# Optimization experiments

Hardware: AMD Instinct MI355X
Metric: run time of the kernel (lower is better)

The kernel has to match this reference:

```python
import jax, jax.numpy as jnp
import numpy as np


def silu(v):
    return v * jax.nn.sigmoid(v)


def setup_inputs() -> dict:
    key = jax.random.key(0)
    ks = jax.random.split(key, 10)
    b, l, d_model = 1, 1024, 1536
    d_inner, dt_rank, d_state, d_conv = 3072, 96, 16, 4
    rn = lambda k, shp, sc: jax.random.normal(k, shp, jnp.float32) * sc
    return {
        "hidden_states": rn(ks[0], (b, l, d_model), 1.0),
        "in_proj_w": rn(ks[1], (2 * d_inner, d_model), 0.02),
        "conv_w": rn(ks[2], (d_inner, d_conv), 0.1),
        "conv_b": rn(ks[3], (d_inner,), 0.1),
        "x_proj_w": rn(ks[4], (dt_rank + 2 * d_state, d_inner), 0.02),
        "dt_proj_w": rn(ks[5], (d_inner, dt_rank), 0.02),
        "dt_proj_b": rn(ks[6], (d_inner,), 0.1),
        "out_proj_w": rn(ks[7], (d_model, d_inner), 0.02),
        "A_log": jnp.log(jax.random.uniform(ks[8], (d_inner, d_state), jnp.float32, 0.5, 8.0)),
        "D": rn(ks[9], (d_inner,), 1.0),
    }


def reference(hidden_states, in_proj_w, conv_w, conv_b, x_proj_w, dt_proj_w, dt_proj_b, out_proj_w, A_log, D):
    b, l, _ = hidden_states.shape
    d_inner, d_conv = conv_w.shape
    dt_rank = dt_proj_w.shape[1]
    d_state = A_log.shape[1]
    negA = -jnp.exp(A_log)  # (d_inner, d_state)

    # in_proj, transpose to channel-major: (b, 2*d_inner, l)
    xz = jnp.einsum('bld,ed->ble', hidden_states, in_proj_w).transpose(0, 2, 1)
    x, z = jnp.split(xz, 2, axis=1)  # each (b, d_inner, l)

    # conv_state = F.pad(x, (d_conv - l, 0)) -> last d_conv columns (l > d_conv)
    conv_state = x[:, :, -d_conv:]

    # causal depthwise conv1d + bias + silu
    xp = jnp.pad(x, ((0, 0), (0, 0), (d_conv - 1, 0)))
    xc = conv_b[None, :, None] + sum(conv_w[None, :, j:j + 1] * xp[:, :, j:j + l] for j in range(d_conv))
    xc = silu(xc)  # (b, d_inner, l)

    # x_proj over channel dim -> dt, B, C
    x_dbl = jnp.einsum('bdl,ed->ble', xc, x_proj_w)  # (b, l, dt_rank+2*d_state)
    dt, Bm, Cm = jnp.split(x_dbl, [dt_rank, dt_rank + d_state], axis=-1)

    # dt_proj (no bias here; bias folded into softplus as delta_bias)
    delta = jax.nn.softplus(jnp.einsum('blr,dr->bdl', dt, dt_proj_w) + dt_proj_b[None, :, None])

    # selective scan: h_t = exp(delta_t * A) * h_{t-1} + delta_t * B_t * x_t
    deltaA = jnp.exp(delta[..., None] * negA[None, :, None, :])          # (b, d, l, n)
    deltaBx = delta[..., None] * Bm[:, None, :, :] * xc[..., None]        # (b, d, l, n)

    def comb(c1, c2):
        a1, u1 = c1
        a2, u2 = c2
        return a1 * a2, a2 * u1 + u2

    _, h = jax.lax.associative_scan(comb, (deltaA, deltaBx), axis=2)      # (b, d, l, n)

    y = jnp.einsum('bdln,bln->bdl', h, Cm) + D[None, :, None] * xc
    y = y * silu(z)

    out = jnp.einsum('bdl,od->blo', y, out_proj_w)  # (b, l, d_model)
    last_state = h[:, :, -1, :]                     # (b, d_inner, d_state)
    return out, conv_state, last_state
```

## Files before the change

kernel.cpp:

```cpp
#include <hip/hip_runtime.h>

using f32x4  = __attribute__((ext_vector_type(4))) float;
using bf16x4 = __attribute__((ext_vector_type(4))) __bf16;
using bf16x8 = __attribute__((ext_vector_type(8))) __bf16;

#define L_SEQ 1024
#define D_MODEL 1536
#define D_INNER 3072
#define DT_RANK 96
#define D_STATE 16

#define SCAN_NC 32
#define SCAN_CL (L_SEQ / SCAN_NC)
#define NCHAIN  (D_INNER * D_STATE)

#define SCRATCH_FLOATS (4 * L_SEQ * D_INNER + L_SEQ * 128 + 3 * SCAN_NC * NCHAIN)
__device__ __align__(16) float g_scratch[SCRATCH_FLOATS];

template <int BM, int BN, int BK, int AMODE, int BMODE, int EPI, int SWZY = 0>
__global__ __launch_bounds__(256) void gemm_bt(
    const float* __restrict__ Ap, const float* __restrict__ Bp,
    float* __restrict__ out0, float* __restrict__ out1,
    const float* __restrict__ bias,
    int M, int N, int K, int lda, int ldb, int ldc)
{
    constexpr int LDSK = BK + 8;
    constexpr int WM = BM / 2, WN = BN / 2;
    constexpr int FM = WM / 16, FN = WN / 16;
    constexpr int CHA = (BM * BK / 256) / 4;
    constexpr int CHB = (BN * BK / 256) / 4;
    constexpr int CPR = BK / 4;
    __shared__ __align__(16) __bf16 As [BM * LDSK];
    __shared__ __align__(16) __bf16 As2[(AMODE == 2) ? BM * LDSK : 8];
    __shared__ __align__(16) __bf16 Bs [BN * LDSK];
    __shared__ __align__(16) __bf16 Bs2[(BMODE == 2) ? BN * LDSK : 8];

    const int tid  = threadIdx.x;
    const int lane = tid & 63;
    const int wid  = tid >> 6;
    const int wm = wid >> 1, wn = wid & 1;

    int m0, n0;
    if constexpr (SWZY > 0) {
        int b   = blockIdx.x;
        int xcd = b & 7;
        int j   = b >> 3;
        m0 = (j / SWZY) * BM;
        n0 = (xcd * SWZY + (j % SWZY)) * BN;
    } else {
        m0 = blockIdx.x * BM;
        n0 = blockIdx.y * BN;
    }

    const int nkt = (K + BK - 1) / BK;
    const int per = (nkt + (int)gridDim.z - 1) / (int)gridDim.z;
    const int kb  = blockIdx.z * per * BK;
    const int ke  = min(K, kb + per * BK);

    f32x4 acc[FM][FN];
#pragma unroll
    for (int i = 0; i < FM; ++i)
#pragma unroll
        for (int j = 0; j < FN; ++j) acc[i][j] = f32x4{0.f, 0.f, 0.f, 0.f};

    const int fr = lane & 15, kq = lane >> 4;

    f32x4 a0[CHA], a1[CHA], b0[CHB], b1[CHB];

    auto loadAb = [&](int kt, f32x4 (&buf)[CHA]) {
#pragma unroll
        for (int i = 0; i < CHA; ++i) {
            int c = i * 256 + tid;
            int r = c / CPR, k4 = c % CPR;
            buf[i] = *(const f32x4*)(Ap + (size_t)(m0 + r) * lda + kt + k4 * 4);
        }
    };
    auto loadBb = [&](int kt, f32x4 (&buf)[CHB]) {
#pragma unroll
        for (int i = 0; i < CHB; ++i) {
            int c = i * 256 + tid;
            int r = c / CPR, k4 = c % CPR;
            buf[i] = *(const f32x4*)(Bp + (size_t)(n0 + r) * ldb + kt + k4 * 4);
        }
    };
    auto writeAb = [&](f32x4 (&buf)[CHA]) {
#pragma unroll
        for (int i = 0; i < CHA; ++i) {
            int c = i * 256 + tid;
            int r = c / CPR, k4 = c % CPR;
            bf16x4 hv;
#pragma unroll
            for (int e = 0; e < 4; ++e) hv[e] = (__bf16)buf[i][e];
            *(bf16x4*)&As[r * LDSK + k4 * 4] = hv;
            if constexpr (AMODE == 2) {
                bf16x4 lv;
#pragma unroll
                for (int e = 0; e < 4; ++e)
                    lv[e] = (__bf16)(buf[i][e] - (float)hv[e]);
                *(bf16x4*)&As2[r * LDSK + k4 * 4] = lv;
            }
        }
    };
    auto writeBb = [&](f32x4 (&buf)[CHB]) {
#pragma unroll
        for (int i = 0; i < CHB; ++i) {
            int c = i * 256 + tid;
            int r = c / CPR, k4 = c % CPR;
            bf16x4 hv;
#pragma unroll
            for (int e = 0; e < 4; ++e) hv[e] = (__bf16)buf[i][e];
            *(bf16x4*)&Bs[r * LDSK + k4 * 4] = hv;
            if constexpr (BMODE == 2) {
                bf16x4 lv;
#pragma unroll
                for (int e = 0; e < 4; ++e)
                    lv[e] = (__bf16)(buf[i][e] - (float)hv[e]);
                *(bf16x4*)&Bs2[r * LDSK + k4 * 4] = lv;
            }
        }
    };
    auto compute = [&]() {
        bf16x8 af[FM], bfg[FN];
#pragma unroll
        for (int fm = 0; fm < FM; ++fm)
            af[fm] = *(const bf16x8*)&As[(wm * WM + fm * 16 + fr) * LDSK + kq * 8];
#pragma unroll
        for (int fn = 0; fn < FN; ++fn)
            bfg[fn] = *(const bf16x8*)&Bs[(wn * WN + fn * 16 + fr) * LDSK + kq * 8];
        if constexpr (AMODE == 2 && BMODE == 2) {
            bf16x8 al[FM], bl[FN];
#pragma unroll
            for (int fm = 0; fm < FM; ++fm)
                al[fm] = *(const bf16x8*)&As2[(wm * WM + fm * 16 + fr) * LDSK + kq * 8];
#pragma unroll
            for (int fn = 0; fn < FN; ++fn)
                bl[fn] = *(const bf16x8*)&Bs2[(wn * WN + fn * 16 + fr) * LDSK + kq * 8];
#pragma unroll
            for (int fm = 0; fm < FM; ++fm)
#pragma unroll
                for (int fn = 0; fn < FN; ++fn) {
                    acc[fm][fn] = __builtin_amdgcn_mfma_f32_16x16x32_bf16(
                        al[fm], bfg[fn], acc[fm][fn], 0, 0, 0);
                    acc[fm][fn] = __builtin_amdgcn_mfma_f32_16x16x32_bf16(
                        af[fm], bl[fn], acc[fm][fn], 0, 0, 0);
                    acc[fm][fn] = __builtin_amdgcn_mfma_f32_16x16x32_bf16(
                        af[fm], bfg[fn], acc[fm][fn], 0, 0, 0);
                }
        } else {
#pragma unroll
            for (int fm = 0; fm < FM; ++fm)
#pragma unroll
                for (int fn = 0; fn < FN; ++fn)
                    acc[fm][fn] = __builtin_amdgcn_mfma_f32_16x16x32_bf16(
                        af[fm], bfg[fn], acc[fm][fn], 0, 0, 0);
        }
    };

    loadAb(kb, a0);
    loadBb(kb, b0);
    if (kb + BK < ke) {
        loadAb(kb + BK, a1);
        loadBb(kb + BK, b1);
    }

    for (int kt = kb; kt < ke; kt += 2 * BK) {
        writeAb(a0);
        writeBb(b0);
        __syncthreads();
        if (kt + 2 * BK < ke) {
            loadAb(kt + 2 * BK, a0);
            loadBb(kt + 2 * BK, b0);
        }
        compute();
        __syncthreads();
        if (kt + BK < ke) {
            writeAb(a1);
            writeBb(b1);
            __syncthreads();
            if (kt + 3 * BK < ke) {
                loadAb(kt + 3 * BK, a1);
                loadBb(kt + 3 * BK, b1);
            }
            compute();
            __syncthreads();
        }
    }

    const int rbase = m0 + wm * WM, cbase = n0 + wn * WN;
#pragma unroll
    for (int fm = 0; fm < FM; ++fm) {
#pragma unroll
        for (int fn = 0; fn < FN; ++fn) {
            int row = rbase + fm * 16 + (lane >> 4) * 4;
            int col = cbase + fn * 16 + (lane & 15);
            f32x4 v = acc[fm][fn];
            if (EPI == 0) {
                int split = N / 2;
                float* d = (col < split) ? out0 : out1;
                int cc = (col < split) ? col : col - split;
#pragma unroll
                for (int j = 0; j < 4; ++j) d[(size_t)(row + j) * ldc + cc] = v[j];
            } else if (EPI == 1) {
                float bz = bias[col];
#pragma unroll
                for (int j = 0; j < 4; ++j) {
                    float t = v[j] + bz;
                    t = (t > 20.f) ? t : log1pf(__expf(t));
                    out0[(size_t)(row + j) * ldc + col] = t;
                }
            } else if (EPI == 2) {
#pragma unroll
                for (int j = 0; j < 4; ++j)
                    atomicAdd(&out0[(size_t)(row + j) * ldc + col], v[j]);
            } else if (EPI == 3) {
#pragma unroll
                for (int j = 0; j < 4; ++j)
                    out0[(size_t)(row + j) * ldc + col] = v[j];
            } else if (EPI == 4) {
                float* d = out0 + (size_t)blockIdx.z * M * ldc;
#pragma unroll
                for (int j = 0; j < 4; ++j)
                    d[(size_t)(row + j) * ldc + col] = v[j];
            } else {
#pragma unroll
                for (int j = 0; j < 4; ++j) {
                    float t = v[j] + bias[row + j];
                    t = (t > 20.f) ? t : log1pf(__expf(t));
                    out0[(size_t)(row + j) * ldc + col] = t;
                }
            }
        }
    }
}

__global__ __launch_bounds__(256) void zero_f32(float* __restrict__ p, int n4)
{
    int i = blockIdx.x * 256 + threadIdx.x;
    if (i < n4) ((f32x4*)p)[i] = f32x4{0.f, 0.f, 0.f, 0.f};
}

__global__ __launch_bounds__(256) void reduce2_f32(
    const float* __restrict__ p, float* __restrict__ out, int n4)
{
    int i = blockIdx.x * 256 + threadIdx.x;
    if (i < n4) {
        f32x4 a = ((const f32x4*)p)[i];
        f32x4 b = ((const f32x4*)(p + (size_t)L_SEQ * D_MODEL))[i];
        ((f32x4*)out)[i] = a + b;
    }
}

__global__ __launch_bounds__(256) void conv_silu(
    const float* __restrict__ x, const float* __restrict__ cw,
    const float* __restrict__ cb, float* __restrict__ xc,
    float* __restrict__ conv_state)
{
    int idx = blockIdx.x * 256 + threadIdx.x;
    int l  = idx / (D_INNER / 4);
    int d4 = (idx % (D_INNER / 4)) * 4;
    const f32x4 zero = f32x4{0.f, 0.f, 0.f, 0.f};
    f32x4 x0 = *(const f32x4*)&x[(size_t)l * D_INNER + d4];
    f32x4 x1 = (l >= 1) ? *(const f32x4*)&x[(size_t)(l - 1) * D_INNER + d4] : zero;
    f32x4 x2 = (l >= 2) ? *(const f32x4*)&x[(size_t)(l - 2) * D_INNER + d4] : zero;
    f32x4 x3 = (l >= 3) ? *(const f32x4*)&x[(size_t)(l - 3) * D_INNER + d4] : zero;
    f32x4 r;
#pragma unroll
    for (int i = 0; i < 4; ++i) {
        int d = d4 + i;
        float w0 = cw[d * 4 + 0], w1 = cw[d * 4 + 1];
        float w2 = cw[d * 4 + 2], w3 = cw[d * 4 + 3];
        float v = cb[d] + w3 * x0[i] + w2 * x1[i] + w1 * x2[i] + w0 * x3[i];
        r[i] = v / (1.f + __expf(-v));
    }
    *(f32x4*)&xc[(size_t)l * D_INNER + d4] = r;
    if (l == L_SEQ - 1) {
#pragma unroll
        for (int i = 0; i < 4; ++i) {
            int d = d4 + i;
            conv_state[d * 4 + 3] = x0[i];
            conv_state[d * 4 + 2] = x1[i];
            conv_state[d * 4 + 1] = x2[i];
            conv_state[d * 4 + 0] = x3[i];
        }
    }
}

__global__ __launch_bounds__(256) void scan_phase1(
    const float* __restrict__ delta, const float* __restrict__ xc,
    const float* __restrict__ dbl, const float* __restrict__ A_log,
    float* __restrict__ U, float* __restrict__ Aprod)
{
    int d = blockIdx.x * 256 + threadIdx.x;
    int c = blockIdx.y;
    float a[D_STATE], h[D_STATE], p[D_STATE];
#pragma unroll
    for (int n = 0; n < D_STATE; n += 4) {
        f32x4 av = *(const f32x4*)&A_log[d * D_STATE + n];
#pragma unroll
        for (int e = 0; e < 4; ++e) {
            a[n + e] = __expf(av[e]);
            h[n + e] = 0.f;
            p[n + e] = 1.f;
        }
    }
    int l0 = c * SCAN_CL;
    for (int i = 0; i < SCAN_CL; ++i) {
        int l = l0 + i;
        float dl = delta[(size_t)l * D_INNER + d];
        float xv = xc[(size_t)l * D_INNER + d];
        const float* Bp = dbl + l * 128 + DT_RANK;
        f32x4 B0 = *(const f32x4*)(Bp);
        f32x4 B1 = *(const f32x4*)(Bp + 4);
        f32x4 B2 = *(const f32x4*)(Bp + 8);
        f32x4 B3 = *(const f32x4*)(Bp + 12);
        float dx = dl * xv;
#pragma unroll
        for (int n = 0; n < D_STATE; ++n) {
            float Bv = (n < 4) ? B0[n] : (n < 8) ? B1[n - 4]
                     : (n < 12) ? B2[n - 8] : B3[n - 12];
            float dA = __expf(-dl * a[n]);
            h[n] = fmaf(dA, h[n], dx * Bv);
            p[n] *= dA;
        }
    }
    size_t base = (size_t)c * NCHAIN + (size_t)d * D_STATE;
#pragma unroll
    for (int n = 0; n < D_STATE; n += 4) {
        *(f32x4*)&U[base + n]     = f32x4{h[n], h[n+1], h[n+2], h[n+3]};
        *(f32x4*)&Aprod[base + n] = f32x4{p[n], p[n+1], p[n+2], p[n+3]};
    }
}

__global__ __launch_bounds__(256) void scan_phase2(
    const float* __restrict__ U, const float* __restrict__ Aprod,
    float* __restrict__ Hin, float* __restrict__ last_state)
{
    int r = blockIdx.x * 256 + threadIdx.x;
    float hin = 0.f;
#pragma unroll
    for (int c = 0; c < SCAN_NC; ++c) {
        Hin[c * NCHAIN + r] = hin;
        hin = fmaf(Aprod[c * NCHAIN + r], hin, U[c * NCHAIN + r]);
    }
    last_state[r] = hin;
}

__global__ __launch_bounds__(256) void scan_phase3(
    const float* __restrict__ delta, const float* __restrict__ xc,
    const float* __restrict__ z, const float* __restrict__ dbl,
    const float* __restrict__ A_log, const float* __restrict__ Dp,
    const float* __restrict__ Hin, float* __restrict__ y)
{
    int d = blockIdx.x * 256 + threadIdx.x;
    int c = blockIdx.y;
    float a[D_STATE], h[D_STATE];
    size_t hbase = (size_t)c * NCHAIN + (size_t)d * D_STATE;
#pragma unroll
    for (int n = 0; n < D_STATE; n += 4) {
        f32x4 av = *(const f32x4*)&A_log[d * D_STATE + n];
        f32x4 hv = *(const f32x4*)&Hin[hbase + n];
#pragma unroll
        for (int e = 0; e < 4; ++e) {
            a[n + e] = __expf(av[e]);
            h[n + e] = hv[e];
        }
    }
    float Dv = Dp[d];
    int l0 = c * SCAN_CL;
    for (int i = 0; i < SCAN_CL; ++i) {
        int l = l0 + i;
        float dl = delta[(size_t)l * D_INNER + d];
        float xv = xc[(size_t)l * D_INNER + d];
        float zv = z[(size_t)l * D_INNER + d];
        const float* Bp = dbl + l * 128 + DT_RANK;
        f32x4 B0 = *(const f32x4*)(Bp);
        f32x4 B1 = *(const f32x4*)(Bp + 4);
        f32x4 B2 = *(const f32x4*)(Bp + 8);
        f32x4 B3 = *(const f32x4*)(Bp + 12);
        f32x4 C0 = *(const f32x4*)(Bp + 16);
        f32x4 C1 = *(const f32x4*)(Bp + 20);
        f32x4 C2 = *(const f32x4*)(Bp + 24);
        f32x4 C3 = *(const f32x4*)(Bp + 28);
        float dx = dl * xv;
        float yv = 0.f;
#pragma unroll
        for (int n = 0; n < D_STATE; ++n) {
            float Bv = (n < 4) ? B0[n] : (n < 8) ? B1[n - 4]
                     : (n < 12) ? B2[n - 8] : B3[n - 12];
            float Cv = (n < 4) ? C0[n] : (n < 8) ? C1[n - 4]
                     : (n < 12) ? C2[n - 8] : C3[n - 12];
            float dA = __expf(-dl * a[n]);
            h[n] = fmaf(dA, h[n], dx * Bv);
            yv = fmaf(h[n], Cv, yv);
        }
        float sz = zv / (1.f + __expf(-zv));
        y[(size_t)l * D_INNER + d] = (yv + Dv * xv) * sz;
    }
}

extern "C" void kernel_launch(void* const* d_in, const int* in_sizes, int n_in,
                              void* d_out, int out_size, void* d_ws, size_t ws_size,
                              hipStream_t stream)
{
    const float* hs    = (const float*)d_in[0];
    const float* Win   = (const float*)d_in[1];
    const float* cw    = (const float*)d_in[2];
    const float* cb    = (const float*)d_in[3];
    const float* Wx    = (const float*)d_in[4];
    const float* Wdt   = (const float*)d_in[5];
    const float* dtb   = (const float*)d_in[6];
    const float* Wout  = (const float*)d_in[7];
    const float* A_log = (const float*)d_in[8];
    const float* Dp    = (const float*)d_in[9];

    float* out        = (float*)d_out;
    float* conv_state = out + (size_t)L_SEQ * D_MODEL;
    float* last_state = conv_state + (size_t)D_INNER * 4;

    const size_t NEED = sizeof(float) * (size_t)SCRATCH_FLOATS;
    float* base;
    if (ws_size >= NEED) {
        base = (float*)d_ws;
    } else {
        void* sp = nullptr;
        hipGetSymbolAddress(&sp, HIP_SYMBOL(g_scratch));
        base = (float*)sp;
    }
    float* buf0 = base;
    float* buf1 = buf0 + (size_t)L_SEQ * D_INNER;
    float* buf2 = buf1 + (size_t)L_SEQ * D_INNER;
    float* buf3 = buf2 + (size_t)L_SEQ * D_INNER;
    float* dbl  = buf3 + (size_t)L_SEQ * D_INNER;
    float* Ubuf = dbl  + (size_t)L_SEQ * 128;
    float* Abuf = Ubuf + (size_t)SCAN_NC * NCHAIN;
    float* Hbuf = Abuf + (size_t)SCAN_NC * NCHAIN;

    zero_f32<<<dim3((L_SEQ * 128 / 4 + 255) / 256), 256, 0, stream>>>(dbl, L_SEQ * 128 / 4);

    gemm_bt<64, 64, 32, 1, 1, 0, 12><<<dim3(1536), 256, 0, stream>>>(
        hs, Win, buf0, buf1, nullptr, L_SEQ, 2 * D_INNER, D_MODEL, D_MODEL, D_MODEL, D_INNER);

    conv_silu<<<dim3(L_SEQ * D_INNER / 4 / 256), 256, 0, stream>>>(buf0, cw, cb, buf2, conv_state);

    gemm_bt<64, 128, 32, 2, 2, 2><<<dim3(16, 1, 24), 256, 0, stream>>>(
        buf2, Wx, dbl, nullptr, nullptr, L_SEQ, 128, D_INNER, D_INNER, D_INNER, 128);

    gemm_bt<64, 64, 32, 2, 2, 1><<<dim3(16, 48), 256, 0, stream>>>(
        dbl, Wdt, buf0, nullptr, dtb, L_SEQ, D_INNER, DT_RANK, 128, DT_RANK, D_INNER);

    scan_phase1<<<dim3(D_INNER / 256, SCAN_NC), 256, 0, stream>>>(
        buf0, buf2, dbl, A_log, Ubuf, Abuf);
    scan_phase2<<<dim3(NCHAIN / 256), 256, 0, stream>>>(
        Ubuf, Abuf, Hbuf, last_state);
    scan_phase3<<<dim3(D_INNER / 256, SCAN_NC), 256, 0, stream>>>(
        buf0, buf2, buf1, dbl, A_log, Dp, Hbuf, buf3);

    gemm_bt<64, 64, 32, 1, 1, 4><<<dim3(16, 24, 2), 256, 0, stream>>>(
        buf3, Wout, buf0, nullptr, nullptr, L_SEQ, D_MODEL, D_INNER, D_INNER, D_INNER, D_MODEL);
    reduce2_f32<<<dim3(L_SEQ * D_MODEL / 4 / 256), 256, 0, stream>>>(
        buf0, out, L_SEQ * D_MODEL / 4);
}
```

Measured before the change: 199.0 us.

## Pre-convert GEMM operands to bf16 and emit scan output in bf16

Adds a kernel that converts hidden_states, in_proj_w and out_proj_w to bf16 on every call. The scan now writes y directly as bf16. The GEMM template gains a mode that loads bf16 tiles straight into shared memory without in-kernel conversion. The in_proj GEMM also switches to a 128x64 tile with half as many blocks. The goal is to halve the global and L2 traffic of the in/out projections and drop per-tile conversion work, at the cost of an extra pass that reads and writes the weights each call.

```diff
diff --git a/kernel.cpp b/kernel.cpp
--- a/kernel.cpp
+++ b/kernel.cpp
@@ -14,12 +14,20 @@
 #define SCAN_CL (L_SEQ / SCAN_NC)
 #define NCHAIN  (D_INNER * D_STATE)
 
-#define SCRATCH_FLOATS (4 * L_SEQ * D_INNER + L_SEQ * 128 + 3 * SCAN_NC * NCHAIN)
+#define HS_Q   (L_SEQ * D_MODEL / 2)
+#define WIN_Q  (2 * D_INNER * D_MODEL / 2)
+#define WOUT_Q (D_MODEL * D_INNER / 2)
+#define Y_Q    (L_SEQ * D_INNER / 2)
+#define SCRATCH_FLOATS (3 * L_SEQ * D_INNER + L_SEQ * 128 + 3 * SCAN_NC * NCHAIN \
+                        + HS_Q + WIN_Q + WOUT_Q + Y_Q)
 __device__ __align__(16) float g_scratch[SCRATCH_FLOATS];
+
+template <bool B16> struct RegT { using T = f32x4; };
+template <> struct RegT<true> { using T = uint4; };
 
 template <int BM, int BN, int BK, int AMODE, int BMODE, int EPI, int SWZY = 0>
 __global__ __launch_bounds__(256) void gemm_bt(
-    const float* __restrict__ Ap, const float* __restrict__ Bp,
+    const void* __restrict__ Ap, const void* __restrict__ Bp,
     float* __restrict__ out0, float* __restrict__ out1,
     const float* __restrict__ bias,
     int M, int N, int K, int lda, int ldb, int ldc)
@@ -27,9 +35,13 @@
     constexpr int LDSK = BK + 8;
     constexpr int WM = BM / 2, WN = BN / 2;
     constexpr int FM = WM / 16, FN = WN / 16;
-    constexpr int CHA = (BM * BK / 256) / 4;
-    constexpr int CHB = (BN * BK / 256) / 4;
-    constexpr int CPR = BK / 4;
+    constexpr int AEPT = (AMODE == 0) ? 8 : 4;
+    constexpr int BEPT = (BMODE == 0) ? 8 : 4;
+    constexpr int CHA = (BM * BK / 256) / AEPT;
+    constexpr int CHB = (BN * BK / 256) / BEPT;
+    constexpr int ACPR = BK / AEPT, BCPR = BK / BEPT;
+    using ART = typename RegT<AMODE == 0>::T;
+    using BRT = typename RegT<BMODE == 0>::T;
     __shared__ __align__(16) __bf16 As [BM * LDSK];
     __shared__ __align__(16) __bf16 As2[(AMODE == 2) ? BM * LDSK : 8];
     __shared__ __align__(16) __bf16 Bs [BN * LDSK];
@@ -65,57 +77,78 @@
 
     const int fr = lane & 15, kq = lane >> 4;
 
-    f32x4 a0[CHA], a1[CHA], b0[CHB], b1[CHB];
-
-    auto loadAb = [&](int kt, f32x4 (&buf)[CHA]) {
+    ART a0[CHA], a1[CHA];
+    BRT b0[CHB], b1[CHB];
+
+    auto loadAb = [&](int kt, ART (&buf)[CHA]) {
 #pragma unroll
         for (int i = 0; i < CHA; ++i) {
             int c = i * 256 + tid;
-            int r = c / CPR, k4 = c % CPR;
-            buf[i] = *(const f32x4*)(Ap + (size_t)(m0 + r) * lda + kt + k4 * 4);
+            int r = c / ACPR, k = c % ACPR;
+            if constexpr (AMODE == 0) {
+                const __bf16* A = (const __bf16*)Ap;
+                buf[i] = *(const uint4*)(A + (size_t)(m0 + r) * lda + kt + k * 8);
+            } else {
+                const float* A = (const float*)Ap;
+                buf[i] = *(const f32x4*)(A + (size_t)(m0 + r) * lda + kt + k * 4);
+            }
         }
     };
-    auto loadBb = [&](int kt, f32x4 (&buf)[CHB]) {
+    auto loadBb = [&](int kt, BRT (&buf)[CHB]) {
 #pragma unroll
         for (int i = 0; i < CHB; ++i) {
             int c = i * 256 + tid;
-            int r = c / CPR, k4 = c % CPR;
-            buf[i] = *(const f32x4*)(Bp + (size_t)(n0 + r) * ldb + kt + k4 * 4);
+            int r = c / BCPR, k = c % BCPR;
+            if constexpr (BMODE == 0) {
+                const __bf16* B = (const __bf16*)Bp;
+                buf[i] = *(const uint4*)(B + (size_t)(n0 + r) * ldb + kt + k * 8);
+            } else {
+                const float* B = (const float*)Bp;
+                buf[i] = *(const f32x4*)(B + (size_t)(n0 + r) * ldb + kt + k * 4);
+            }
         }
     };
-    auto writeAb = [&](f32x4 (&buf)[CHA]) {
+    auto writeAb = [&](ART (&buf)[CHA]) {
 #pragma unroll
         for (int i = 0; i < CHA; ++i) {
             int c = i * 256 + tid;
-            int r = c / CPR, k4 = c % CPR;
-            bf16x4 hv;
-#pragma unroll
-            for (int e = 0; e < 4; ++e) hv[e] = (__bf16)buf[i][e];
-            *(bf16x4*)&As[r * LDSK + k4 * 4] = hv;
-            if constexpr (AMODE == 2) {
-                bf16x4 lv;
-#pragma unroll
-                for (int e = 0; e < 4; ++e)
-                    lv[e] = (__bf16)(buf[i][e] - (float)hv[e]);
-                *(bf16x4*)&As2[r * LDSK + k4 * 4] = lv;
+            int r = c / ACPR, k = c % ACPR;
+            if constexpr (AMODE == 0) {
+                *(uint4*)&As[r * LDSK + k * 8] = buf[i];
+            } else {
+                bf16x4 hv;
+#pragma unroll
+                for (int e = 0; e < 4; ++e) hv[e] = (__bf16)buf[i][e];
+                *(bf16x4*)&As[r * LDSK + k * 4] = hv;
+                if constexpr (AMODE == 2) {
+                    bf16x4 lv;
+#pragma unroll
+                    for (int e = 0; e < 4; ++e)
+                        lv[e] = (__bf16)(buf[i][e] - (float)hv[e]);
+                    *(bf16x4*)&As2[r * LDSK + k * 4] = lv;
+                }
             }
         }
     };
-    auto writeBb = [&](f32x4 (&buf)[CHB]) {
+    auto writeBb = [&](BRT (&buf)[CHB]) {
 #pragma unroll
         for (int i = 0; i < CHB; ++i) {
             int c = i * 256 + tid;
-            int r = c / CPR, k4 = c % CPR;
-            bf16x4 hv;
-#pragma unroll
-            for (int e = 0; e < 4; ++e) hv[e] = (__bf16)buf[i][e];
-            *(bf16x4*)&Bs[r * LDSK + k4 * 4] = hv;
-            if constexpr (BMODE == 2) {
-                bf16x4 lv;
-#pragma unroll
-                for (int e = 0; e < 4; ++e)
-                    lv[e] = (__bf16)(buf[i][e] - (float)hv[e]);
-                *(bf16x4*)&Bs2[r * LDSK + k4 * 4] = lv;
+            int r = c / BCPR, k = c % BCPR;
+            if constexpr (BMODE == 0) {
+                *(uint4*)&Bs[r * LDSK + k * 8] = buf[i];
+            } else {
+                bf16x4 hv;
+#pragma unroll
+                for (int e = 0; e < 4; ++e) hv[e] = (__bf16)buf[i][e];
+                *(bf16x4*)&Bs[r * LDSK + k * 4] = hv;
+                if constexpr (BMODE == 2) {
+                    bf16x4 lv;
+#pragma unroll
+                    for (int e = 0; e < 4; ++e)
+                        lv[e] = (__bf16)(buf[i][e] - (float)hv[e]);
+                    *(bf16x4*)&Bs2[r * LDSK + k * 4] = lv;
+                }
             }
         }
     };
@@ -239,6 +272,24 @@
     if (i < n4) ((f32x4*)p)[i] = f32x4{0.f, 0.f, 0.f, 0.f};
 }
 
+__global__ __launch_bounds__(256) void cvt3_bf16(
+    const float* __restrict__ s0, __bf16* __restrict__ d0, int n0q,
+    const float* __restrict__ s1, __bf16* __restrict__ d1, int n1q,
+    const float* __restrict__ s2, __bf16* __restrict__ d2, int n2q)
+{
+    int i = blockIdx.x * 256 + threadIdx.x;
+    const float* s; __bf16* d; int q;
+    if (i < n0q) { s = s0; d = d0; q = i; }
+    else if (i < n0q + n1q) { s = s1; d = d1; q = i - n0q; }
+    else if (i < n0q + n1q + n2q) { s = s2; d = d2; q = i - n0q - n1q; }
+    else return;
+    f32x4 v = ((const f32x4*)s)[q];
+    bf16x4 o;
+#pragma unroll
+    for (int e = 0; e < 4; ++e) o[e] = (__bf16)v[e];
+    ((bf16x4*)d)[q] = o;
+}
+
 __global__ __launch_bounds__(256) void reduce2_f32(
     const float* __restrict__ p, float* __restrict__ out, int n4)
 {
@@ -349,7 +400,7 @@
     const float* __restrict__ delta, const float* __restrict__ xc,
     const float* __restrict__ z, const float* __restrict__ dbl,
     const float* __restrict__ A_log, const float* __restrict__ Dp,
-    const float* __restrict__ Hin, float* __restrict__ y)
+    const float* __restrict__ Hin, __bf16* __restrict__ y)
 {
     int d = blockIdx.x * 256 + threadIdx.x;
     int c = blockIdx.y;
@@ -394,7 +445,7 @@
             yv = fmaf(h[n], Cv, yv);
         }
         float sz = zv / (1.f + __expf(-zv));
-        y[(size_t)l * D_INNER + d] = (yv + Dv * xv) * sz;
+        y[(size_t)l * D_INNER + d] = (__bf16)((yv + Dv * xv) * sz);
     }
 }
 
@@ -429,16 +480,27 @@
     float* buf0 = base;
     float* buf1 = buf0 + (size_t)L_SEQ * D_INNER;
     float* buf2 = buf1 + (size_t)L_SEQ * D_INNER;
-    float* buf3 = buf2 + (size_t)L_SEQ * D_INNER;
-    float* dbl  = buf3 + (size_t)L_SEQ * D_INNER;
+    float* dbl  = buf2 + (size_t)L_SEQ * D_INNER;
     float* Ubuf = dbl  + (size_t)L_SEQ * 128;
     float* Abuf = Ubuf + (size_t)SCAN_NC * NCHAIN;
     float* Hbuf = Abuf + (size_t)SCAN_NC * NCHAIN;
-
+    __bf16* hsB   = (__bf16*)(Hbuf + (size_t)SCAN_NC * NCHAIN);
+    __bf16* WinB  = hsB  + (size_t)L_SEQ * D_MODEL;
+    __bf16* WoutB = WinB + (size_t)2 * D_INNER * D_MODEL;
+    __bf16* yB    = WoutB + (size_t)D_MODEL * D_INNER;
+
+    {
+        int q0 = L_SEQ * D_MODEL / 4;
+        int q1 = 2 * D_INNER * D_MODEL / 4;
+        int q2 = D_MODEL * D_INNER / 4;
+        int nb = (q0 + q1 + q2 + 255) / 256;
+        cvt3_bf16<<<dim3(nb), 256, 0, stream>>>(hs, hsB, q0, Win, WinB, q1,
+                                                Wout, WoutB, q2);
+    }
     zero_f32<<<dim3((L_SEQ * 128 / 4 + 255) / 256), 256, 0, stream>>>(dbl, L_SEQ * 128 / 4);
 
-    gemm_bt<64, 64, 32, 1, 1, 0, 12><<<dim3(1536), 256, 0, stream>>>(
-        hs, Win, buf0, buf1, nullptr, L_SEQ, 2 * D_INNER, D_MODEL, D_MODEL, D_MODEL, D_INNER);
+    gemm_bt<128, 64, 32, 0, 0, 0, 12><<<dim3(768), 256, 0, stream>>>(
+        hsB, WinB, buf0, buf1, nullptr, L_SEQ, 2 * D_INNER, D_MODEL, D_MODEL, D_MODEL, D_INNER);
 
     conv_silu<<<dim3(L_SEQ * D_INNER / 4 / 256), 256, 0, stream>>>(buf0, cw, cb, buf2, conv_state);
 
@@ -453,10 +515,10 @@
     scan_phase2<<<dim3(NCHAIN / 256), 256, 0, stream>>>(
         Ubuf, Abuf, Hbuf, last_state);
     scan_phase3<<<dim3(D_INNER / 256, SCAN_NC), 256, 0, stream>>>(
-        buf0, buf2, buf1, dbl, A_log, Dp, Hbuf, buf3);
-
-    gemm_bt<64, 64, 32, 1, 1, 4><<<dim3(16, 24, 2), 256, 0, stream>>>(
-        buf3, Wout, buf0, nullptr, nullptr, L_SEQ, D_MODEL, D_INNER, D_INNER, D_INNER, D_MODEL);
+        buf0, buf2, buf1, dbl, A_log, Dp, Hbuf, yB);
+
+    gemm_bt<64, 64, 32, 0, 0, 4><<<dim3(16, 24, 2), 256, 0, stream>>>(
+        yB, WoutB, buf0, nullptr, nullptr, L_SEQ, D_MODEL, D_INNER, D_INNER, D_INNER, D_MODEL);
     reduce2_f32<<<dim3(L_SEQ * D_MODEL / 4 / 256), 256, 0, stream>>>(
         buf0, out, L_SEQ * D_MODEL / 4);
 }
```

Result: slower. 242.6 us (+21.9%).
